# Kernel tuning notes

Hardware: AMD Instinct MI355X
Metric: run time of the kernel (lower is better)

## Reference

```python
import jax, jax.numpy as jnp
import numpy as np

B, N, DIM, H = 8, 1024, 768, 12
D = DIM // H
SCALE = D ** -0.5
EPS = 1e-5


def setup_inputs() -> dict:
    key = jax.random.key(0)
    ks = jax.random.split(key, 6)
    s = 0.02
    return {
        "x": jax.random.normal(ks[0], (B, N, DIM), jnp.float32),
        "w_qv": jax.random.normal(ks[1], (2 * DIM, DIM), jnp.float32) * s,
        "ext_k": jax.random.normal(ks[2], (1, H, N, D), jnp.float32),
        "ext_bias": jax.random.normal(ks[3], (1, H, N, N), jnp.float32),
        "bn_gamma": jnp.ones((H,), jnp.float32),
        "bn_beta": jnp.zeros((H,), jnp.float32),
        "w_proj": jax.random.normal(ks[4], (DIM, DIM), jnp.float32) * s,
        "b_proj": jnp.zeros((DIM,), jnp.float32),
    }


def reference(x, w_qv, ext_k, ext_bias, bn_gamma, bn_beta, w_proj, b_proj):
    b, n, c = x.shape
    # qv projection (no bias), split into q and v
    qv = jnp.einsum('bnc,ec->bne', x, w_qv)  # [B,N,2C]
    q, v = jnp.split(qv, 2, axis=-1)
    # b n (h d) -> b h n d
    q = q.reshape(b, n, H, D).transpose(0, 2, 1, 3)
    v = v.reshape(b, n, H, D).transpose(0, 2, 1, 3)
    # scores: (q @ ext_k^T + bias) * scale  -> [B,H,N,N]
    attn = (jnp.einsum('bhnd,xhmd->bhnm', q, ext_k) + ext_bias) * SCALE
    # BatchNorm2d over heads (training-mode batch stats over B,N,N)
    mean = jnp.mean(attn, axis=(0, 2, 3), keepdims=True)
    var = jnp.mean(jnp.square(attn - mean), axis=(0, 2, 3), keepdims=True)
    attn = (attn - mean) * jax.lax.rsqrt(var + EPS)
    attn = attn * bn_gamma[None, :, None, None] + bn_beta[None, :, None, None]
    # softmax over keys, dropout p=0
    attn = jax.nn.softmax(attn, axis=-1)
    out = jnp.einsum('bhnm,bhmd->bhnd', attn, v)
    out = out.transpose(0, 2, 1, 3).reshape(b, n, c)  # b h n d -> b n (h d)
    return jnp.einsum('bnc,oc->bno', out, w_proj) + b_proj
```

## Files before the change

kernel.cpp:

```cpp
#include <hip/hip_runtime.h>
#include <cstdint>

#define B_    8
#define N_    1024
#define DIM_  768
#define H_    12
#define D_    64
#define SCALE_ 0.125f
#define GQ_   32
#define GK_   4

typedef unsigned short u16;
typedef short bf16x8 __attribute__((ext_vector_type(8)));
typedef float f32x4  __attribute__((ext_vector_type(4)));

__device__ __forceinline__ u16 f2b(float f) {
  union { float f; unsigned u; } v; v.f = f;
  unsigned r = v.u + 0x7FFFu + ((v.u >> 16) & 1u);
  return (u16)(r >> 16);
}
__device__ __forceinline__ u16 phu(float f) {
  union { float f; unsigned u; } v; v.f = f;
  return (u16)((v.u + 0x8000u) >> 16);
}
__device__ __forceinline__ float b2f(u16 h) {
  union { unsigned u; float f; } v; v.u = ((unsigned)h) << 16; return v.f;
}
#if __has_builtin(__builtin_amdgcn_exp2f)
__device__ __forceinline__ float exp2fast(float x) { return __builtin_amdgcn_exp2f(x); }
#else
__device__ __forceinline__ float exp2fast(float x) { return __expf(x * 0.69314718f); }
#endif
__device__ __forceinline__ void gl2lds16(const void* g, void* l) {
  __builtin_amdgcn_global_load_lds(
      (const __attribute__((address_space(1))) void*)g,
      (__attribute__((address_space(3))) void*)l, 16, 0, 0);
}

__global__ __launch_bounds__(256) void cast_all(
    const float4* __restrict__ s0, u16* __restrict__ d0, int n0,
    const float4* __restrict__ s1, u16* __restrict__ d1, int n1,
    const float4* __restrict__ s2, u16* __restrict__ d2, int n2,
    const float4* __restrict__ s3, u16* __restrict__ d3, int n3)
{
  int i = blockIdx.x * 256 + threadIdx.x;
  const float4* s; u16* d; int off;
  if (i < n0)               { s = s0; d = d0; off = i; }
  else if (i < n0+n1)       { s = s1; d = d1; off = i - n0; }
  else if (i < n0+n1+n2)    { s = s2; d = d2; off = i - n0 - n1; }
  else if (i < n0+n1+n2+n3) { s = s3; d = d3; off = i - n0 - n1 - n2; }
  else return;
  float4 v = s[off];
  ushort4 o; o.x = f2b(v.x); o.y = f2b(v.y); o.z = f2b(v.z); o.w = f2b(v.w);
  *(ushort4*)(d + (size_t)off * 4) = o;
}

__global__ __launch_bounds__(256) void qv_gemm(
    const u16* __restrict__ A, const u16* __restrict__ W,
    u16* __restrict__ qo, u16* __restrict__ vo)
{
  __shared__ u16 As[128*32];
  __shared__ u16 Bs[128*32];
  const int tid = threadIdx.x, lane = tid & 63, wid = tid >> 6;
  const int m0 = blockIdx.y * 128, n0 = blockIdx.x * 128;
  const int wm = (wid >> 1) * 64, wn = (wid & 1) * 64;
  const int lr = lane & 15, lq = lane >> 4;
  f32x4 acc[4][4] = {};
  for (int k0 = 0; k0 < 768; k0 += 32) {
#pragma unroll
    for (int it = 0; it < 2; ++it) {
      int c = it * 256 + tid;
      int row = c >> 2, c8 = c & 3;
      gl2lds16(A + (size_t)(m0 + row) * 768 + k0 + c8 * 8, (char*)As + (it*256 + wid*64) * 16);
      gl2lds16(W + (size_t)(n0 + row) * 768 + k0 + c8 * 8, (char*)Bs + (it*256 + wid*64) * 16);
    }
    __syncthreads();
    bf16x8 af[4], bfr[4];
#pragma unroll
    for (int i = 0; i < 4; ++i) {
      af[i]  = *(const bf16x8*)&As[(wm + i*16 + lr) * 32 + lq * 8];
      bfr[i] = *(const bf16x8*)&Bs[(wn + i*16 + lr) * 32 + lq * 8];
    }
#pragma unroll
    for (int mi = 0; mi < 4; ++mi)
#pragma unroll
      for (int nj = 0; nj < 4; ++nj)
        acc[mi][nj] = __builtin_amdgcn_mfma_f32_16x16x32_bf16(af[mi], bfr[nj], acc[mi][nj], 0, 0, 0);
    __syncthreads();
  }
#pragma unroll
  for (int mi = 0; mi < 4; ++mi)
#pragma unroll
    for (int nj = 0; nj < 4; ++nj)
#pragma unroll
      for (int r = 0; r < 4; ++r) {
        int row = m0 + wm + mi*16 + lq*4 + r;
        int col = n0 + wn + nj*16 + lr;
        u16 bv = f2b(acc[mi][nj][r]);
        int b = row >> 10, n = row & 1023;
        if (col < 768) { int h = col >> 6, d = col & 63;
          qo[(((size_t)(b*12 + h)) << 16) + (n << 6) + d] = bv;
        } else { int e = col - 768; int h = e >> 6, d = e & 63;
          vo[(((size_t)(b*12 + h)) << 16) + (n << 6) + d] = bv;
        }
      }
}

__global__ __launch_bounds__(256) void transpose_v(
    const u16* __restrict__ v, u16* __restrict__ vt,
    const u16* __restrict__ kk, u16* __restrict__ ktT)
{
  __shared__ u16 t[64][65];
  int y = blockIdx.y, n0 = blockIdx.x * 64, tid = threadIdx.x;
  const u16* src; u16* dst;
  if (y < 96) { src = v  + (((size_t)y) << 16) + (size_t)n0 * 64;      dst = vt  + (((size_t)y) << 16) + n0; }
  else { int h = y - 96; src = kk + (((size_t)h) << 16) + (size_t)n0 * 64; dst = ktT + (((size_t)h) << 16) + n0; }
#pragma unroll
  for (int i = 0; i < 16; ++i) {
    int e = i*256 + tid; t[e >> 6][e & 63] = src[e];
  }
  __syncthreads();
#pragma unroll
  for (int i = 0; i < 16; ++i) {
    int e = i*256 + tid; int d = e >> 6, r = e & 63;
    dst[(size_t)d * 1024 + r] = t[r][d];
  }
}

__global__ __launch_bounds__(256) void qs_kernel(const u16* __restrict__ q, float* __restrict__ qs)
{
  int idx = blockIdx.x * 256 + threadIdx.x;
  int h = idx >> 16, rem = idx & 65535;
  float s = 0.f;
#pragma unroll
  for (int b = 0; b < 8; ++b) s += b2f(q[(((size_t)(b*12 + h)) << 16) + rem]);
  qs[idx] = s;
}

__global__ __launch_bounds__(256) void gram_kernel(
    const u16* __restrict__ src, float* __restrict__ gpart,
    int rows_per_block, int b_interleaved)
{
  __shared__ float t[64*68];
  const int h = blockIdx.y, r0 = blockIdx.x * rows_per_block, tid = threadIdx.x;
  const int rr = (tid >> 4) * 4;
  const int cc = (tid & 15) * 4;
  float a[4][4] = {{0.f}};
  for (int t0 = 0; t0 < rows_per_block; t0 += 64) {
#pragma unroll
    for (int i = 0; i < 4; ++i) {
      int e = i*256 + tid;
      int r = e >> 4, d4 = (e & 15) * 4;
      int gr = r0 + t0 + r;
      size_t addr;
      if (b_interleaved) { int b = gr >> 10, n = gr & 1023;
        addr = (((size_t)(b*12 + h)) << 16) + (n << 6) + d4; }
      else addr = (((size_t)h) << 16) + ((size_t)gr << 6) + d4;
      ushort4 u = *(const ushort4*)(src + addr);
      float4 f; f.x = b2f(u.x); f.y = b2f(u.y); f.z = b2f(u.z); f.w = b2f(u.w);
      *(float4*)&t[r*68 + d4] = f;
    }
    __syncthreads();
#pragma unroll 4
    for (int m = 0; m < 64; ++m) {
      float4 rv = *(const float4*)&t[m*68 + rr];
      float4 cv = *(const float4*)&t[m*68 + cc];
      a[0][0] += rv.x*cv.x; a[0][1] += rv.x*cv.y; a[0][2] += rv.x*cv.z; a[0][3] += rv.x*cv.w;
      a[1][0] += rv.y*cv.x; a[1][1] += rv.y*cv.y; a[1][2] += rv.y*cv.z; a[1][3] += rv.y*cv.w;
      a[2][0] += rv.z*cv.x; a[2][1] += rv.z*cv.y; a[2][2] += rv.z*cv.z; a[2][3] += rv.z*cv.w;
      a[3][0] += rv.w*cv.x; a[3][1] += rv.w*cv.y; a[3][2] += rv.w*cv.z; a[3][3] += rv.w*cv.w;
    }
    __syncthreads();
  }
  float* g = gpart + (((size_t)blockIdx.x) * 12 + h) * 4096;
#pragma unroll
  for (int i = 0; i < 4; ++i)
    *(float4*)&g[(rr + i)*64 + cc] = make_float4(a[i][0], a[i][1], a[i][2], a[i][3]);
}

__global__ __launch_bounds__(256) void bias_stats(
    const float* __restrict__ bias, const u16* __restrict__ ktT,
    const float* __restrict__ qs, float* __restrict__ acc)
{
  __shared__ float red[12];
  const int tid = threadIdx.x, lane = tid & 63, wid = tid >> 6;
  const int lr = lane & 15, lq = lane >> 4;
  const int h = blockIdx.y;
  const int nb = blockIdx.x & 15, mb = blockIdx.x >> 4;
  const int n0 = nb * 64 + wid * 16;
  const size_t brow = (((size_t)h) << 20) + ((size_t)(n0 + lr) << 10);
  const size_t kbase = ((size_t)h) << 16;
  f32x4 kb[4] = {};
  float sb = 0.f, sb2 = 0.f;
#pragma unroll
  for (int ms = 0; ms < 4; ++ms) {
    const int m0 = mb * 256 + ms * 64;
#pragma unroll
    for (int ks = 0; ks < 2; ++ks) {
      const int mc = m0 + ks * 32 + lq * 8;
      float4 b0 = *(const float4*)(bias + brow + mc);
      float4 b1 = *(const float4*)(bias + brow + mc + 4);
      sb  += b0.x + b0.y + b0.z + b0.w + b1.x + b1.y + b1.z + b1.w;
      sb2 += b0.x*b0.x + b0.y*b0.y + b0.z*b0.z + b0.w*b0.w
           + b1.x*b1.x + b1.y*b1.y + b1.z*b1.z + b1.w*b1.w;
      union { bf16x8 v; u16 u[8]; } af;
      af.u[0] = f2b(b0.x); af.u[1] = f2b(b0.y); af.u[2] = f2b(b0.z); af.u[3] = f2b(b0.w);
      af.u[4] = f2b(b1.x); af.u[5] = f2b(b1.y); af.u[6] = f2b(b1.z); af.u[7] = f2b(b1.w);
#pragma unroll
      for (int dj = 0; dj < 4; ++dj) {
        bf16x8 bfr = *(const bf16x8*)(ktT + kbase + (size_t)(dj*16 + lr) * 1024 + mc);
        kb[dj] = __builtin_amdgcn_mfma_f32_16x16x32_bf16(af.v, bfr, kb[dj], 0, 0, 0);
      }
    }
  }
  float cross = 0.f;
#pragma unroll
  for (int dj = 0; dj < 4; ++dj)
#pragma unroll
    for (int r = 0; r < 4; ++r)
      cross += kb[dj][r] *
               qs[kbase + ((size_t)(nb*64 + wid*16 + lq*4 + r) << 6) + dj*16 + lr];
#pragma unroll
  for (int s = 32; s; s >>= 1) {
    sb += __shfl_xor(sb, s); sb2 += __shfl_xor(sb2, s); cross += __shfl_xor(cross, s);
  }
  if (lane == 0) { red[wid] = sb; red[4 + wid] = sb2; red[8 + wid] = cross; }
  __syncthreads();
  if (tid == 0) {
    atomicAdd(acc + h,      red[0] + red[1] + red[2] + red[3]);
    atomicAdd(acc + 12 + h, red[4] + red[5] + red[6] + red[7]);
    atomicAdd(acc + 24 + h, red[8] + red[9] + red[10] + red[11]);
  }
}

__global__ __launch_bounds__(256) void sums_kernel(
    const float* __restrict__ qs, const u16* __restrict__ kb16,
    float* __restrict__ qsum, float* __restrict__ ksum)
{
  __shared__ float red[256];
  int h = blockIdx.x, yc = blockIdx.y;
  int tid = threadIdx.x, d = tid & 63, qq = tid >> 6;
  if (yc < 8) {
    float s = 0.f;
    int nbase = yc * 128 + qq * 32;
    for (int n = 0; n < 32; ++n)
      s += qs[(((size_t)h) << 16) + ((size_t)(nbase + n) << 6) + d];
    red[tid] = s; __syncthreads();
    if (qq == 0) atomicAdd(&qsum[h*64 + d], red[d] + red[64+d] + red[128+d] + red[192+d]);
  } else {
    float s = 0.f;
    int nbase = qq * 256;
    for (int n = 0; n < 256; ++n)
      s += b2f(kb16[(((size_t)h) << 16) + ((size_t)(nbase + n) << 6) + d]);
    red[tid] = s; __syncthreads();
    if (qq == 0) ksum[h*64 + d] = red[d] + red[64+d] + red[128+d] + red[192+d];
  }
}

__global__ __launch_bounds__(256) void finalize_kernel(
    const float* __restrict__ qsum, const float* __restrict__ ksum,
    const float* __restrict__ Qgp, const float* __restrict__ Kgp,
    const float* __restrict__ acc, const float* __restrict__ gamma,
    float* __restrict__ temp)
{
  __shared__ float qg[4096];
  __shared__ float kg[4096];
  __shared__ float red[8];
  int h = blockIdx.x, tid = threadIdx.x, wid = tid >> 6, lane = tid & 63;
#pragma unroll
  for (int i = 0; i < 16; ++i) {
    int e = i*256 + tid;
    float q = 0.f, k = 0.f;
    for (int g = 0; g < GQ_; ++g) q += Qgp[(((size_t)g)*12 + h)*4096 + e];
#pragma unroll
    for (int g = 0; g < GK_; ++g) k += Kgp[(((size_t)g)*12 + h)*4096 + e];
    qg[e] = q; kg[e] = k;
  }
  __syncthreads();
  float s2 = 0.f;
#pragma unroll
  for (int i = 0; i < 16; ++i) { int e = i*256 + tid; s2 += qg[e]*kg[e]; }
  float s1 = (tid < 64) ? qsum[h*64 + tid] * ksum[h*64 + tid] : 0.f;
#pragma unroll
  for (int s = 32; s; s >>= 1) { s2 += __shfl_xor(s2, s); s1 += __shfl_xor(s1, s); }
  if (lane == 0) { red[wid] = s2; red[4 + wid] = s1; }
  __syncthreads();
  if (tid == 0) {
    double S2 = (double)red[0] + red[1] + red[2] + red[3];
    double S1 = (double)red[4];
    double M = 8388608.0;
    double Sb = acc[h], Sb2 = acc[12 + h], Cross = acc[24 + h];
    double Eraw  = (S1 + 8.0 * Sb) / M;
    double Eraw2 = (S2 + 2.0 * Cross + 8.0 * Sb2) / M;
    double var = (double)SCALE_ * (double)SCALE_ * (Eraw2 - Eraw * Eraw);
    double rstd = 1.0 / sqrt(var + 1e-5);
    temp[h] = (float)((double)gamma[h] * (double)SCALE_ * rstd);
  }
}

__global__ __launch_bounds__(256) void attn_kernel(
    const u16* __restrict__ q, const u16* __restrict__ k, const u16* __restrict__ vT,
    const float* __restrict__ bias, const float* __restrict__ temp, u16* __restrict__ out)
{
  __shared__ u16 kt[4096];
  __shared__ u16 vt[5120];
  __shared__ u16 pt[128*72];
  const int tid = threadIdx.x, lane = tid & 63, wid = tid >> 6;
  const int lr = lane & 15, lq = lane >> 4;
  const int X = blockIdx.x;
  const int g = X >> 6, r_ = X & 63, b = r_ >> 3, q8 = r_ & 7;
  const int p = g*8 + q8;
  const int h = p % 12, n0 = (p / 12) * 128;
  const size_t qbase = ((((size_t)b) * 12 + h) << 16) + ((size_t)n0 << 6);
  const size_t kbase = ((size_t)h) << 16;
  const size_t vbase = ((((size_t)b) * 12 + h) << 16);
  const size_t bbase = (((size_t)h) << 20) + ((size_t)n0 << 10);
  const float tmp2 = temp[h] * 1.44269504f;
  const int W = wid * 32;

  bf16x8 aq[2][2];
#pragma unroll
  for (int mi = 0; mi < 2; ++mi)
#pragma unroll
    for (int ks = 0; ks < 2; ++ks)
      aq[mi][ks] = *(const bf16x8*)(q + qbase + (size_t)(W + mi*16 + lr)*64 + ks*32 + lq*8);

  for (int i = tid; i < 1024; i += 256) {
    int ks = i >> 9, rr = (i >> 5) & 15, cc = i & 31;
    vt[ks*2560 + (64 + rr)*32 + cc] = (rr == 0) ? (u16)0x3F80 : (u16)0;
  }

  const float* br[2][4];
#pragma unroll
  for (int mi = 0; mi < 2; ++mi)
#pragma unroll
    for (int r = 0; r < 4; ++r)
      br[mi][r] = bias + bbase + (size_t)(W + mi*16 + lq*4 + r) * 1024 + lr;

  f32x4 oacc[5][2] = {};

  for (int m0 = 0; m0 < 1024; m0 += 64) {
#pragma unroll
    for (int it = 0; it < 2; ++it) {
      int c = it*256 + tid; int ks = c >> 8, r = (c >> 2) & 63, c8 = c & 3;
      gl2lds16(k  + kbase + (size_t)(m0 + r) * 64 + ks*32 + c8*8, (char*)kt + (it*256 + wid*64) * 16);
      gl2lds16(vT + vbase + (size_t)r * 1024 + m0 + ks*32 + c8*8, (char*)vt + it*5120 + wid*1024);
    }
    f32x4 s[2][4];
#pragma unroll
    for (int mi = 0; mi < 2; ++mi)
#pragma unroll
      for (int nj = 0; nj < 4; ++nj)
#pragma unroll
        for (int r = 0; r < 4; ++r)
          s[mi][nj][r] = br[mi][r][m0 + nj*16];
    __syncthreads();
#pragma unroll
    for (int ks = 0; ks < 2; ++ks) {
#pragma unroll
      for (int nj = 0; nj < 4; ++nj) {
        bf16x8 bk = *(const bf16x8*)&kt[ks*2048 + (nj*16 + lr)*32 + lq*8];
#pragma unroll
        for (int mi = 0; mi < 2; ++mi)
          s[mi][nj] = __builtin_amdgcn_mfma_f32_16x16x32_bf16(aq[mi][ks], bk, s[mi][nj], 0, 0, 0);
      }
    }
#pragma unroll
    for (int mi = 0; mi < 2; ++mi)
#pragma unroll
      for (int r = 0; r < 4; ++r) {
        int row = W + mi*16 + lq*4 + r;
#pragma unroll
        for (int nj = 0; nj < 4; ++nj)
          pt[row*72 + nj*16 + lr] = phu(exp2fast(s[mi][nj][r] * tmp2));
      }
#pragma unroll
    for (int ks = 0; ks < 2; ++ks) {
      bf16x8 bp[2];
#pragma unroll
      for (int ni = 0; ni < 2; ++ni)
        bp[ni] = *(const bf16x8*)&pt[(W + ni*16 + lr)*72 + ks*32 + lq*8];
#pragma unroll
      for (int dj = 0; dj < 5; ++dj) {
        bf16x8 av = *(const bf16x8*)&vt[ks*2560 + (dj*16 + lr)*32 + lq*8];
#pragma unroll
        for (int ni = 0; ni < 2; ++ni)
          oacc[dj][ni] = __builtin_amdgcn_mfma_f32_16x16x32_bf16(av, bp[ni], oacc[dj][ni], 0, 0, 0);
      }
    }
    __syncthreads();
  }
#pragma unroll
  for (int ni = 0; ni < 2; ++ni) {
    float l = __shfl(oacc[4][ni][0], lr);
    float linv = __builtin_amdgcn_rcpf(l);
    int n = n0 + W + ni*16 + lr;
    u16* orow = out + (size_t)(b*1024 + n) * 768 + h*64 + lq*4;
#pragma unroll
    for (int dj = 0; dj < 4; ++dj) {
      ushort4 o;
      o.x = f2b(oacc[dj][ni][0] * linv); o.y = f2b(oacc[dj][ni][1] * linv);
      o.z = f2b(oacc[dj][ni][2] * linv); o.w = f2b(oacc[dj][ni][3] * linv);
      *(ushort4*)(orow + dj*16) = o;
    }
  }
}

__global__ __launch_bounds__(256) void proj_gemm(
    const u16* __restrict__ A, const u16* __restrict__ W,
    const float* __restrict__ bp, float* __restrict__ out)
{
  __shared__ u16 As[128*32];
  __shared__ u16 Bs[128*32];
  const int tid = threadIdx.x, lane = tid & 63, wid = tid >> 6;
  const int m0 = blockIdx.y * 128, n0 = blockIdx.x * 128;
  const int wm = (wid >> 1) * 64, wn = (wid & 1) * 64;
  const int lr = lane & 15, lq = lane >> 4;
  f32x4 acc[4][4] = {};
  for (int k0 = 0; k0 < 768; k0 += 32) {
#pragma unroll
    for (int it = 0; it < 2; ++it) {
      int c = it*256 + tid; int row = c >> 2, c8 = c & 3;
      gl2lds16(A + (size_t)(m0 + row) * 768 + k0 + c8*8, (char*)As + (it*256 + wid*64) * 16);
      gl2lds16(W + (size_t)(n0 + row) * 768 + k0 + c8*8, (char*)Bs + (it*256 + wid*64) * 16);
    }
    __syncthreads();
    bf16x8 af[4], bfr[4];
#pragma unroll
    for (int i = 0; i < 4; ++i) {
      af[i]  = *(const bf16x8*)&As[(wm + i*16 + lr)*32 + lq*8];
      bfr[i] = *(const bf16x8*)&Bs[(wn + i*16 + lr)*32 + lq*8];
    }
#pragma unroll
    for (int mi = 0; mi < 4; ++mi)
#pragma unroll
      for (int nj = 0; nj < 4; ++nj)
        acc[mi][nj] = __builtin_amdgcn_mfma_f32_16x16x32_bf16(af[mi], bfr[nj], acc[mi][nj], 0, 0, 0);
    __syncthreads();
  }
#pragma unroll
  for (int mi = 0; mi < 4; ++mi)
#pragma unroll
    for (int nj = 0; nj < 4; ++nj)
#pragma unroll
      for (int r = 0; r < 4; ++r) {
        int row = m0 + wm + mi*16 + lq*4 + r;
        int col = n0 + wn + nj*16 + lr;
        out[(size_t)row * 768 + col] = acc[mi][nj][r] + bp[col];
      }
}

extern "C" void kernel_launch(void* const* d_in, const int* in_sizes, int n_in,
                              void* d_out, int out_size, void* d_ws, size_t ws_size,
                              hipStream_t stream)
{
  const float* x     = (const float*)d_in[0];
  const float* wqv   = (const float*)d_in[1];
  const float* ek    = (const float*)d_in[2];
  const float* ebias = (const float*)d_in[3];
  const float* gamma = (const float*)d_in[4];
  const float* wp    = (const float*)d_in[6];
  const float* bp    = (const float*)d_in[7];
  float* out = (float*)d_out;

  char* ws = (char*)d_ws;
  size_t off = 0;
  auto alloc = [&](size_t bytes) { char* p = ws + off; off += (bytes + 255) & ~(size_t)255; return p; };
  u16* x16   = (u16*)alloc((size_t)8192*768*2);
  u16* wqv16 = (u16*)alloc((size_t)1536*768*2);
  u16* wp16  = (u16*)alloc((size_t)768*768*2);
  u16* k16   = (u16*)alloc((size_t)12*1024*64*2);
  u16* ktT16 = (u16*)alloc((size_t)12*64*1024*2);
  u16* q16   = (u16*)alloc((size_t)8*12*1024*64*2);
  u16* v16   = (u16*)alloc((size_t)8*12*1024*64*2);
  u16* vt16  = (u16*)alloc((size_t)8*12*1024*64*2);
  float* qs  = (float*)alloc((size_t)12*1024*64*4);
  float* acc = (float*)alloc(3*12*4);
  float* qsum = (float*)alloc(12*64*4);
  float* ksum = (float*)alloc(12*64*4);
  size_t zbytes = (size_t)(((char*)ksum + 12*64*4) - (char*)acc);
  float* temp = (float*)alloc(12*4);
  float* Qgp = (float*)x16;
  float* Kgp = Qgp + (size_t)GQ_*12*4096;
  u16* attn16 = x16;

  hipMemsetAsync(acc, 0, zbytes, stream);

  {
    int c0 = 8192*768/4, c1 = 1536*768/4, c2 = 768*768/4, c3 = 12*1024*64/4;
    int total = c0 + c1 + c2 + c3;
    cast_all<<<(total + 255)/256, 256, 0, stream>>>(
        (const float4*)x, x16, c0, (const float4*)wqv, wqv16, c1,
        (const float4*)wp, wp16, c2, (const float4*)ek, k16, c3);
  }
  qv_gemm<<<dim3(12, 64), 256, 0, stream>>>(x16, wqv16, q16, v16);
  transpose_v<<<dim3(16, 108), 256, 0, stream>>>(v16, vt16, k16, ktT16);
  qs_kernel<<<3072, 256, 0, stream>>>(q16, qs);
  gram_kernel<<<dim3(GK_, 12), 256, 0, stream>>>(k16, Kgp, 1024/GK_, 0);
  gram_kernel<<<dim3(GQ_, 12), 256, 0, stream>>>(q16, Qgp, 8192/GQ_, 1);
  bias_stats<<<dim3(64, 12), 256, 0, stream>>>(ebias, ktT16, qs, acc);
  sums_kernel<<<dim3(12, 9), 256, 0, stream>>>(qs, k16, qsum, ksum);
  finalize_kernel<<<12, 256, 0, stream>>>(qsum, ksum, Qgp, Kgp, acc, gamma, temp);
  attn_kernel<<<dim3(768), 256, 0, stream>>>(q16, k16, vt16, ebias, temp, attn16);
  proj_gemm<<<dim3(6, 64), 256, 0, stream>>>(attn16, wp16, bp, out);
}
```

Measured before the change: 310.6 us.

## Fuse transposes and stats kernels, write V transposed from GEMM epilogue

The qv GEMM epilogue now writes V directly in transposed layout, and the cast kernel writes the transposed ext_k copy and zeroes the accumulators, which removes the transpose kernel and the memset. The qs, sums and both gram kernels are merged into one stats_fused launch that also accumulates qsum. The aim is to cut launch count and extra memory passes. In exchange the transposed stores are strided and uncoalesced (ushort4 for V, scattered u16 for K).

```diff
diff --git a/kernel.cpp b/kernel.cpp
--- a/kernel.cpp
+++ b/kernel.cpp
@@ -41,23 +41,33 @@
     const float4* __restrict__ s0, u16* __restrict__ d0, int n0,
     const float4* __restrict__ s1, u16* __restrict__ d1, int n1,
     const float4* __restrict__ s2, u16* __restrict__ d2, int n2,
-    const float4* __restrict__ s3, u16* __restrict__ d3, int n3)
-{
-  int i = blockIdx.x * 256 + threadIdx.x;
-  const float4* s; u16* d; int off;
-  if (i < n0)               { s = s0; d = d0; off = i; }
-  else if (i < n0+n1)       { s = s1; d = d1; off = i - n0; }
-  else if (i < n0+n1+n2)    { s = s2; d = d2; off = i - n0 - n1; }
-  else if (i < n0+n1+n2+n3) { s = s3; d = d3; off = i - n0 - n1 - n2; }
+    const float4* __restrict__ s3, u16* __restrict__ d3, int n3,
+    u16* __restrict__ ktT, float* __restrict__ zptr, int zfloats)
+{
+  const int tid = threadIdx.x;
+  if (blockIdx.x == 0)
+    for (int j = tid; j < zfloats; j += 256) zptr[j] = 0.f;
+  int i = blockIdx.x * 256 + tid;
+  const float4* s; u16* d; int off; int br;
+  if (i < n0)               { s = s0; d = d0; off = i; br = 0; }
+  else if (i < n0+n1)       { s = s1; d = d1; off = i - n0; br = 1; }
+  else if (i < n0+n1+n2)    { s = s2; d = d2; off = i - n0 - n1; br = 2; }
+  else if (i < n0+n1+n2+n3) { s = s3; d = d3; off = i - n0 - n1 - n2; br = 3; }
   else return;
   float4 v = s[off];
   ushort4 o; o.x = f2b(v.x); o.y = f2b(v.y); o.z = f2b(v.z); o.w = f2b(v.w);
   *(ushort4*)(d + (size_t)off * 4) = o;
+  if (br == 3) {
+    int flat = off * 4;
+    int h = flat >> 16, rem = flat & 65535, n = rem >> 6, d4 = rem & 63;
+    u16* kb = ktT + (h << 16) + (d4 << 10) + n;
+    kb[0] = o.x; kb[1024] = o.y; kb[2048] = o.z; kb[3072] = o.w;
+  }
 }
 
 __global__ __launch_bounds__(256) void qv_gemm(
     const u16* __restrict__ A, const u16* __restrict__ W,
-    u16* __restrict__ qo, u16* __restrict__ vo)
+    u16* __restrict__ qo, u16* __restrict__ vto)
 {
   __shared__ u16 As[128*32];
   __shared__ u16 Bs[128*32];
@@ -88,94 +98,101 @@
         acc[mi][nj] = __builtin_amdgcn_mfma_f32_16x16x32_bf16(af[mi], bfr[nj], acc[mi][nj], 0, 0, 0);
     __syncthreads();
   }
-#pragma unroll
-  for (int mi = 0; mi < 4; ++mi)
-#pragma unroll
-    for (int nj = 0; nj < 4; ++nj)
-#pragma unroll
-      for (int r = 0; r < 4; ++r) {
-        int row = m0 + wm + mi*16 + lq*4 + r;
-        int col = n0 + wn + nj*16 + lr;
-        u16 bv = f2b(acc[mi][nj][r]);
-        int b = row >> 10, n = row & 1023;
-        if (col < 768) { int h = col >> 6, d = col & 63;
-          qo[(((size_t)(b*12 + h)) << 16) + (n << 6) + d] = bv;
-        } else { int e = col - 768; int h = e >> 6, d = e & 63;
-          vo[(((size_t)(b*12 + h)) << 16) + (n << 6) + d] = bv;
+  if (n0 < 768) {
+#pragma unroll
+    for (int mi = 0; mi < 4; ++mi)
+#pragma unroll
+      for (int nj = 0; nj < 4; ++nj)
+#pragma unroll
+        for (int r = 0; r < 4; ++r) {
+          int row = m0 + wm + mi*16 + lq*4 + r;
+          int col = n0 + wn + nj*16 + lr;
+          int b = row >> 10, n = row & 1023;
+          int h = col >> 6, d = col & 63;
+          qo[(((size_t)(b*12 + h)) << 16) + (n << 6) + d] = f2b(acc[mi][nj][r]);
         }
-      }
-}
-
-__global__ __launch_bounds__(256) void transpose_v(
-    const u16* __restrict__ v, u16* __restrict__ vt,
-    const u16* __restrict__ kk, u16* __restrict__ ktT)
-{
-  __shared__ u16 t[64][65];
-  int y = blockIdx.y, n0 = blockIdx.x * 64, tid = threadIdx.x;
-  const u16* src; u16* dst;
-  if (y < 96) { src = v  + (((size_t)y) << 16) + (size_t)n0 * 64;      dst = vt  + (((size_t)y) << 16) + n0; }
-  else { int h = y - 96; src = kk + (((size_t)h) << 16) + (size_t)n0 * 64; dst = ktT + (((size_t)h) << 16) + n0; }
-#pragma unroll
-  for (int i = 0; i < 16; ++i) {
-    int e = i*256 + tid; t[e >> 6][e & 63] = src[e];
-  }
-  __syncthreads();
-#pragma unroll
-  for (int i = 0; i < 16; ++i) {
-    int e = i*256 + tid; int d = e >> 6, r = e & 63;
-    dst[(size_t)d * 1024 + r] = t[r][d];
-  }
-}
-
-__global__ __launch_bounds__(256) void qs_kernel(const u16* __restrict__ q, float* __restrict__ qs)
-{
-  int idx = blockIdx.x * 256 + threadIdx.x;
-  int h = idx >> 16, rem = idx & 65535;
-  float s = 0.f;
-#pragma unroll
-  for (int b = 0; b < 8; ++b) s += b2f(q[(((size_t)(b*12 + h)) << 16) + rem]);
-  qs[idx] = s;
-}
-
-__global__ __launch_bounds__(256) void gram_kernel(
-    const u16* __restrict__ src, float* __restrict__ gpart,
-    int rows_per_block, int b_interleaved)
+  } else {
+#pragma unroll
+    for (int mi = 0; mi < 4; ++mi)
+#pragma unroll
+      for (int nj = 0; nj < 4; ++nj) {
+        int rowb = m0 + wm + mi*16 + lq*4;
+        int b = rowb >> 10, n = rowb & 1023;
+        int e = n0 + wn + nj*16 + lr - 768;
+        int h = e >> 6, d = e & 63;
+        ushort4 o;
+        o.x = f2b(acc[mi][nj][0]); o.y = f2b(acc[mi][nj][1]);
+        o.z = f2b(acc[mi][nj][2]); o.w = f2b(acc[mi][nj][3]);
+        *(ushort4*)(vto + (((size_t)(b*12 + h)) << 16) + (d << 10) + n) = o;
+      }
+  }
+}
+
+__global__ __launch_bounds__(256) void stats_fused(
+    const u16* __restrict__ q, const u16* __restrict__ k,
+    float* __restrict__ qs, float* __restrict__ qsum, float* __restrict__ ksum,
+    float* __restrict__ Kgp, float* __restrict__ Qgp)
 {
   __shared__ float t[64*68];
-  const int h = blockIdx.y, r0 = blockIdx.x * rows_per_block, tid = threadIdx.x;
-  const int rr = (tid >> 4) * 4;
-  const int cc = (tid & 15) * 4;
-  float a[4][4] = {{0.f}};
-  for (int t0 = 0; t0 < rows_per_block; t0 += 64) {
-#pragma unroll
-    for (int i = 0; i < 4; ++i) {
-      int e = i*256 + tid;
-      int r = e >> 4, d4 = (e & 15) * 4;
-      int gr = r0 + t0 + r;
-      size_t addr;
-      if (b_interleaved) { int b = gr >> 10, n = gr & 1023;
-        addr = (((size_t)(b*12 + h)) << 16) + (n << 6) + d4; }
-      else addr = (((size_t)h) << 16) + ((size_t)gr << 6) + d4;
-      ushort4 u = *(const ushort4*)(src + addr);
-      float4 f; f.x = b2f(u.x); f.y = b2f(u.y); f.z = b2f(u.z); f.w = b2f(u.w);
-      *(float4*)&t[r*68 + d4] = f;
-    }
-    __syncthreads();
+  const int h = blockIdx.y, bx = blockIdx.x, tid = threadIdx.x;
+  if (bx < 16) {
+    const int n0b = bx * 64, d = tid & 63, rg = tid >> 6;
+    float part = 0.f;
+    for (int i = 0; i < 16; ++i) {
+      int n = n0b + rg + 4*i;
+      float s = 0.f;
+#pragma unroll
+      for (int b = 0; b < 8; ++b)
+        s += b2f(q[(((size_t)(b*12 + h)) << 16) + (n << 6) + d]);
+      qs[(((size_t)h) << 16) + (n << 6) + d] = s;
+      part += s;
+    }
+    t[tid] = part; __syncthreads();
+    if (rg == 0) atomicAdd(&qsum[h*64 + d], t[d] + t[64+d] + t[128+d] + t[192+d]);
+  } else if (bx == 16) {
+    const int d = tid & 63, rg = tid >> 6;
+    float s = 0.f;
+    for (int n = rg; n < 1024; n += 4)
+      s += b2f(k[(((size_t)h) << 16) + (n << 6) + d]);
+    t[tid] = s; __syncthreads();
+    if (rg == 0) ksum[h*64 + d] = t[d] + t[64+d] + t[128+d] + t[192+d];
+  } else {
+    const int isQ = (bx >= 21);
+    const int gx = isQ ? (bx - 21) : (bx - 17);
+    const int r0 = gx * 256;
+    const int rr = (tid >> 4) * 4, cc = (tid & 15) * 4;
+    const u16* src = isQ ? q : k;
+    float a[4][4] = {{0.f}};
+    for (int t0 = 0; t0 < 256; t0 += 64) {
+#pragma unroll
+      for (int i = 0; i < 4; ++i) {
+        int e = i*256 + tid; int r = e >> 4, d4 = (e & 15) * 4;
+        int gr = r0 + t0 + r;
+        size_t addr;
+        if (isQ) { int b = gr >> 10, n = gr & 1023;
+          addr = (((size_t)(b*12 + h)) << 16) + (n << 6) + d4; }
+        else addr = (((size_t)h) << 16) + ((size_t)gr << 6) + d4;
+        ushort4 u = *(const ushort4*)(src + addr);
+        float4 f; f.x = b2f(u.x); f.y = b2f(u.y); f.z = b2f(u.z); f.w = b2f(u.w);
+        *(float4*)&t[r*68 + d4] = f;
+      }
+      __syncthreads();
 #pragma unroll 4
-    for (int m = 0; m < 64; ++m) {
-      float4 rv = *(const float4*)&t[m*68 + rr];
-      float4 cv = *(const float4*)&t[m*68 + cc];
-      a[0][0] += rv.x*cv.x; a[0][1] += rv.x*cv.y; a[0][2] += rv.x*cv.z; a[0][3] += rv.x*cv.w;
-      a[1][0] += rv.y*cv.x; a[1][1] += rv.y*cv.y; a[1][2] += rv.y*cv.z; a[1][3] += rv.y*cv.w;
-      a[2][0] += rv.z*cv.x; a[2][1] += rv.z*cv.y; a[2][2] += rv.z*cv.z; a[2][3] += rv.z*cv.w;
-      a[3][0] += rv.w*cv.x; a[3][1] += rv.w*cv.y; a[3][2] += rv.w*cv.z; a[3][3] += rv.w*cv.w;
-    }
-    __syncthreads();
-  }
-  float* g = gpart + (((size_t)blockIdx.x) * 12 + h) * 4096;
-#pragma unroll
-  for (int i = 0; i < 4; ++i)
-    *(float4*)&g[(rr + i)*64 + cc] = make_float4(a[i][0], a[i][1], a[i][2], a[i][3]);
+      for (int m = 0; m < 64; ++m) {
+        float4 rv = *(const float4*)&t[m*68 + rr];
+        float4 cv = *(const float4*)&t[m*68 + cc];
+        a[0][0] += rv.x*cv.x; a[0][1] += rv.x*cv.y; a[0][2] += rv.x*cv.z; a[0][3] += rv.x*cv.w;
+        a[1][0] += rv.y*cv.x; a[1][1] += rv.y*cv.y; a[1][2] += rv.y*cv.z; a[1][3] += rv.y*cv.w;
+        a[2][0] += rv.z*cv.x; a[2][1] += rv.z*cv.y; a[2][2] += rv.z*cv.z; a[2][3] += rv.z*cv.w;
+        a[3][0] += rv.w*cv.x; a[3][1] += rv.w*cv.y; a[3][2] += rv.w*cv.z; a[3][3] += rv.w*cv.w;
+      }
+      __syncthreads();
+    }
+    float* g = (isQ ? Qgp : Kgp) + (((size_t)gx) * 12 + h) * 4096;
+#pragma unroll
+    for (int i = 0; i < 4; ++i)
+      *(float4*)&g[(rr + i)*64 + cc] = make_float4(a[i][0], a[i][1], a[i][2], a[i][3]);
+  }
 }
 
 __global__ __launch_bounds__(256) void bias_stats(
@@ -230,30 +247,6 @@
     atomicAdd(acc + h,      red[0] + red[1] + red[2] + red[3]);
     atomicAdd(acc + 12 + h, red[4] + red[5] + red[6] + red[7]);
     atomicAdd(acc + 24 + h, red[8] + red[9] + red[10] + red[11]);
-  }
-}
-
-__global__ __launch_bounds__(256) void sums_kernel(
-    const float* __restrict__ qs, const u16* __restrict__ kb16,
-    float* __restrict__ qsum, float* __restrict__ ksum)
-{
-  __shared__ float red[256];
-  int h = blockIdx.x, yc = blockIdx.y;
-  int tid = threadIdx.x, d = tid & 63, qq = tid >> 6;
-  if (yc < 8) {
-    float s = 0.f;
-    int nbase = yc * 128 + qq * 32;
-    for (int n = 0; n < 32; ++n)
-      s += qs[(((size_t)h) << 16) + ((size_t)(nbase + n) << 6) + d];
-    red[tid] = s; __syncthreads();
-    if (qq == 0) atomicAdd(&qsum[h*64 + d], red[d] + red[64+d] + red[128+d] + red[192+d]);
-  } else {
-    float s = 0.f;
-    int nbase = qq * 256;
-    for (int n = 0; n < 256; ++n)
-      s += b2f(kb16[(((size_t)h) << 16) + ((size_t)(nbase + n) << 6) + d]);
-    red[tid] = s; __syncthreads();
-    if (qq == 0) ksum[h*64 + d] = red[d] + red[64+d] + red[128+d] + red[192+d];
   }
 }
 
@@ -472,34 +465,28 @@
   u16* k16   = (u16*)alloc((size_t)12*1024*64*2);
   u16* ktT16 = (u16*)alloc((size_t)12*64*1024*2);
   u16* q16   = (u16*)alloc((size_t)8*12*1024*64*2);
-  u16* v16   = (u16*)alloc((size_t)8*12*1024*64*2);
   u16* vt16  = (u16*)alloc((size_t)8*12*1024*64*2);
   float* qs  = (float*)alloc((size_t)12*1024*64*4);
   float* acc = (float*)alloc(3*12*4);
   float* qsum = (float*)alloc(12*64*4);
   float* ksum = (float*)alloc(12*64*4);
-  size_t zbytes = (size_t)(((char*)ksum + 12*64*4) - (char*)acc);
+  int zfloats = (int)(((size_t)(((char*)ksum + 12*64*4) - (char*)acc)) / 4);
   float* temp = (float*)alloc(12*4);
   float* Qgp = (float*)x16;
   float* Kgp = Qgp + (size_t)GQ_*12*4096;
   u16* attn16 = x16;
-
-  hipMemsetAsync(acc, 0, zbytes, stream);
 
   {
     int c0 = 8192*768/4, c1 = 1536*768/4, c2 = 768*768/4, c3 = 12*1024*64/4;
     int total = c0 + c1 + c2 + c3;
     cast_all<<<(total + 255)/256, 256, 0, stream>>>(
         (const float4*)x, x16, c0, (const float4*)wqv, wqv16, c1,
-        (const float4*)wp, wp16, c2, (const float4*)ek, k16, c3);
-  }
-  qv_gemm<<<dim3(12, 64), 256, 0, stream>>>(x16, wqv16, q16, v16);
-  transpose_v<<<dim3(16, 108), 256, 0, stream>>>(v16, vt16, k16, ktT16);
-  qs_kernel<<<3072, 256, 0, stream>>>(q16, qs);
-  gram_kernel<<<dim3(GK_, 12), 256, 0, stream>>>(k16, Kgp, 1024/GK_, 0);
-  gram_kernel<<<dim3(GQ_, 12), 256, 0, stream>>>(q16, Qgp, 8192/GQ_, 1);
+        (const float4*)wp, wp16, c2, (const float4*)ek, k16, c3,
+        ktT16, acc, zfloats);
+  }
+  qv_gemm<<<dim3(12, 64), 256, 0, stream>>>(x16, wqv16, q16, vt16);
+  stats_fused<<<dim3(53, 12), 256, 0, stream>>>(q16, k16, qs, qsum, ksum, Kgp, Qgp);
   bias_stats<<<dim3(64, 12), 256, 0, stream>>>(ebias, ktT16, qs, acc);
-  sums_kernel<<<dim3(12, 9), 256, 0, stream>>>(qs, k16, qsum, ksum);
   finalize_kernel<<<12, 256, 0, stream>>>(qsum, ksum, Qgp, Kgp, acc, gamma, temp);
   attn_kernel<<<dim3(768), 256, 0, stream>>>(q16, k16, vt16, ebias, temp, attn16);
   proj_gemm<<<dim3(6, 64), 256, 0, stream>>>(attn16, wp16, bp, out);
```

Measured after the change: 334.2 us. 1.08x slower.
